# Kernel tuning notes

Measured on AMD Instinct MI355X. Metric: run time of the kernel, lower is better.

The kernel has to match this reference:

```python
import jax, jax.numpy as jnp
import numpy as np

H = 16      # q heads
G = 4       # groups (n_rep)
THETA = 10000.0


def _rope(x, cos, sin):
    # x pairs adjacent elements (torch complex view of reshape(..., -1, 2))
    x0 = x[..., ::2]
    x1 = x[..., 1::2]
    r0 = x0 * cos - x1 * sin
    r1 = x0 * sin + x1 * cos
    return jnp.stack([r0, r1], axis=-1).reshape(x.shape)


def setup_inputs() -> dict:
    key = jax.random.key(0)
    ks = jax.random.split(key, 5)
    B, S, D = 2, 2048, 1024
    return {
        "x": jax.random.normal(ks[0], (B, S, D), jnp.float32),
        "Wq": jax.random.normal(ks[1], (D, D), jnp.float32) * 0.02,
        "Wk": jax.random.normal(ks[2], (D, D // G), jnp.float32) * 0.02,
        "Wv": jax.random.normal(ks[3], (D, D // G), jnp.float32) * 0.02,
        "Wo": jax.random.normal(ks[4], (D, D), jnp.float32) * 0.02,
    }


def reference(x, Wq, Wk, Wv, Wo):
    B, S, D = x.shape
    hd = D // H                     # head dim = 64
    Hkv = H // G                    # kv heads = 4

    q = x @ Wq                      # (B,S,D)
    k = x @ Wk                      # (B,S,D/G)
    v = x @ Wv                      # (B,S,D/G)

    # repeat_kv: (B,S,Hkv,hd) -> (B,S,H,hd)
    k = jnp.repeat(k.reshape(B, S, Hkv, hd), G, axis=2)
    v = jnp.repeat(v.reshape(B, S, Hkv, hd), G, axis=2)

    # RoPE angles: freqs precomputed over hidden_dim (as in source)
    inv = 1.0 / (THETA ** (jnp.arange(0, D, 2, dtype=jnp.float32) / D))  # (D/2,)
    ang = jnp.arange(S, dtype=jnp.float32)[:, None] * inv[None, :]       # (S,D/2)
    q = _rope(q, jnp.cos(ang)[None], jnp.sin(ang)[None])                 # (B,S,D)
    angk = ang[:, : hd // 2]                                             # (S,hd/2)
    k = _rope(k, jnp.cos(angk)[None, :, None, :], jnp.sin(angk)[None, :, None, :])

    q = q.reshape(B, S, H, hd).transpose(0, 2, 1, 3)   # (B,H,S,hd)
    k = k.transpose(0, 2, 1, 3)
    v = v.transpose(0, 2, 1, 3)

    # NOTE: scale uses sqrt(hidden_dim), faithful to source
    scores = jnp.einsum('bhqd,bhkd->bhqk', q, k) / jnp.sqrt(jnp.float32(D))
    p = jax.nn.softmax(scores, axis=-1)
    o = jnp.einsum('bhqk,bhkd->bhqd', p, v)
    o = o.transpose(0, 2, 1, 3).reshape(B, S, D)
    return o @ Wo
```

## Files before the change

### kernel.cpp

```cpp
#include <hip/hip_runtime.h>
#include <math.h>

#define BATCH 2
#define SEQ   2048
#define DMODEL 1024
#define KDIM  1024
#define NH    16
#define HDIM  64
#define GRP   4
#define NKV   4
#define NSPLIT 2

enum { M_PLAIN = 0, M_QKV = 1 };

#define LN_THETA 9.210340371976184f
#define QSCALE 0.04508422002778f

typedef short bf8_t __attribute__((ext_vector_type(8)));
typedef float f4_t __attribute__((ext_vector_type(4)));
typedef unsigned short us4_t __attribute__((ext_vector_type(4)));
typedef unsigned short us8_t __attribute__((ext_vector_type(8)));
typedef _Float16 h_t;
typedef _Float16 h4_t __attribute__((ext_vector_type(4)));

#define QB_OFF 0
#define KB_OFF 4194304
#define VB_OFF (4194304 + 1048576)

__device__ __forceinline__ unsigned short f2bf(float f) {
  unsigned int u = __float_as_uint(f);
  u += 0x7fffu + ((u >> 16) & 1u);
  return (unsigned short)(u >> 16);
}

__device__ __forceinline__ float fexp2(float x) {
#if __has_builtin(__builtin_amdgcn_exp2f)
  return __builtin_amdgcn_exp2f(x);
#else
  return exp2f(x);
#endif
}

__device__ __forceinline__ void gload_lds16(const void* g, void* l) {
  typedef __attribute__((address_space(1))) unsigned int gu32;
  typedef __attribute__((address_space(3))) unsigned int lu32;
  __builtin_amdgcn_global_load_lds((const gu32*)g, (lu32*)l, 16, 0, 0);
}

__global__ __launch_bounds__(256) void conv_x(const float* __restrict__ in,
                                              unsigned short* __restrict__ out) {
  const int i = blockIdx.x * 256 + threadIdx.x;
  float4 v = ((const float4*)in)[i];
  us4_t o = {f2bf(v.x), f2bf(v.y), f2bf(v.z), f2bf(v.w)};
  ((us4_t*)out)[i] = o;
}

__global__ __launch_bounds__(256) void convT_all(const float* __restrict__ W0,
                                                 const float* __restrict__ W1,
                                                 const float* __restrict__ W2,
                                                 const float* __restrict__ W3,
                                                 unsigned short* __restrict__ Wqkvt,
                                                 unsigned short* __restrict__ Wot) {
  const float* W; unsigned short* out; int N, rowoff;
  switch (blockIdx.z) {
    case 0: W = W0; out = Wqkvt; N = 1024; rowoff = 0;    break;
    case 1: W = W1; out = Wqkvt; N = 256;  rowoff = 1024; break;
    case 2: W = W2; out = Wqkvt; N = 256;  rowoff = 1280; break;
    default: W = W3; out = Wot;  N = 1024; rowoff = 0;    break;
  }
  const int n0 = blockIdx.x * 64;
  if (n0 >= N) return;
  __shared__ unsigned short T[64][72];
  const int t = threadIdx.x;
  const int k0 = blockIdx.y * 64;
  const int kr = t >> 4, n4 = (t & 15) * 4;
#pragma unroll
  for (int i = 0; i < 4; ++i) {
    const int k = kr + i * 16;
    float4 v = *(const float4*)&W[(size_t)(k0 + k) * N + n0 + n4];
    T[n4 + 0][k] = f2bf(v.x);
    T[n4 + 1][k] = f2bf(v.y);
    T[n4 + 2][k] = f2bf(v.z);
    T[n4 + 3][k] = f2bf(v.w);
  }
  __syncthreads();
#pragma unroll
  for (int i = 0; i < 2; ++i) {
    const int c = t + i * 256;
    const int n = c >> 3, kc = (c & 7) * 8;
    us8_t v = *(const us8_t*)&T[n][kc];
    *(us8_t*)&out[(size_t)(rowoff + n0 + n) * KDIM + k0 + kc] = v;
  }
}

template <int MODE>
__global__ __launch_bounds__(512, 2) void gemm_bf16(const unsigned short* __restrict__ A,
                                                    const unsigned short* __restrict__ Bt,
                                                    void* __restrict__ Cdst_, int N) {
  __shared__ __align__(16) unsigned short As[4 * 4096];
  __shared__ __align__(16) unsigned short Bs[4 * 4096];

  const int tid = threadIdx.x;
  const int lane = tid & 63, quad = lane >> 4, l16 = lane & 15;
  const int w = tid >> 6, wm = w >> 1, wn = w & 1;
  const int row0 = blockIdx.x * 128, col0 = blockIdx.y * 128;

  const int m0 = tid >> 2;
  const int kc0 = (tid & 3) ^ ((m0 >> 1) & 3);
  const unsigned short* Ag0 = A + (size_t)(row0 + m0) * KDIM + kc0 * 8;
  const unsigned short* Bg0 = Bt + (size_t)(col0 + m0) * KDIM + kc0 * 8;
  unsigned short* Al0 = &As[tid * 8];
  unsigned short* Bl0 = &Bs[tid * 8];

#define STAGE_GEMM(kk)                                          \
  do {                                                          \
    _Pragma("unroll") for (int kh = 0; kh < 4; ++kh) {          \
      gload_lds16(Ag0 + (kk) + kh * 32, Al0 + kh * 4096);       \
      gload_lds16(Bg0 + (kk) + kh * 32, Bl0 + kh * 4096);       \
    }                                                           \
  } while (0)

  int aoff[2][4], boff[4][4];
#pragma unroll
  for (int mi = 0; mi < 2; ++mi) {
    const int am = wm * 32 + mi * 16 + l16;
    const int sw = quad ^ ((am >> 1) & 3);
#pragma unroll
    for (int kh = 0; kh < 4; ++kh)
      aoff[mi][kh] = kh * 4096 + (((am << 2) | sw) << 3);
  }
#pragma unroll
  for (int ni = 0; ni < 4; ++ni) {
    const int bn = wn * 64 + ni * 16 + l16;
    const int sw = quad ^ ((bn >> 1) & 3);
#pragma unroll
    for (int kh = 0; kh < 4; ++kh)
      boff[ni][kh] = kh * 4096 + (((bn << 2) | sw) << 3);
  }

  f4_t acc[2][4];
#pragma unroll
  for (int mi = 0; mi < 2; ++mi)
#pragma unroll
    for (int ni = 0; ni < 4; ++ni) acc[mi][ni] = (f4_t){0.f, 0.f, 0.f, 0.f};

  for (int kb = 0; kb < KDIM; kb += 128) {
    __syncthreads();
    STAGE_GEMM(kb);
    __syncthreads();

#pragma unroll
    for (int kh = 0; kh < 4; ++kh) {
      bf8_t af[2], bfr[4];
#pragma unroll
      for (int mi = 0; mi < 2; ++mi) af[mi] = *(const bf8_t*)&As[aoff[mi][kh]];
#pragma unroll
      for (int ni = 0; ni < 4; ++ni) bfr[ni] = *(const bf8_t*)&Bs[boff[ni][kh]];
#pragma unroll
      for (int mi = 0; mi < 2; ++mi)
#pragma unroll
        for (int ni = 0; ni < 4; ++ni)
          acc[mi][ni] = __builtin_amdgcn_mfma_f32_16x16x32_bf16(af[mi], bfr[ni], acc[mi][ni], 0, 0, 0);
    }
  }
#undef STAGE_GEMM

  if constexpr (MODE == M_PLAIN) {
    float* out = (float*)Cdst_;
#pragma unroll
    for (int mi = 0; mi < 2; ++mi) {
      const int rowb = row0 + wm * 32 + mi * 16 + quad * 4;
#pragma unroll
      for (int ni = 0; ni < 4; ++ni) {
        const int n = col0 + wn * 64 + ni * 16 + l16;
#pragma unroll
        for (int r = 0; r < 4; ++r)
          out[(size_t)(rowb + r) * N + n] = acc[mi][ni][r];
      }
    }
  } else {
    unsigned short* Qb = (unsigned short*)Cdst_;
    unsigned short* Kb = Qb + (KB_OFF - QB_OFF);
    unsigned short* Vb = Qb + (VB_OFF - QB_OFF);
#pragma unroll
    for (int ni = 0; ni < 4; ++ni) {
      const int nb = col0 + wn * 64 + ni * 16;
      const int n = nb + l16;
      if (nb < 1024) {
        const float inv = expf(-(float)(2 * (n >> 1)) * (LN_THETA / (float)DMODEL));
        const float sgn = (n & 1) ? 1.f : -1.f;
        const int h = n >> 6, d = n & 63;
#pragma unroll
        for (int mi = 0; mi < 2; ++mi) {
          const int rowb = row0 + wm * 32 + mi * 16 + quad * 4;
#pragma unroll
          for (int r = 0; r < 4; ++r) {
            const int row = rowb + r;
            const int bb = row >> 11, s = row & (SEQ - 1);
            const float v = acc[mi][ni][r];
            const float p = __shfl_xor(v, 1);
            float sn, cs;
            sincosf((float)s * inv, &sn, &cs);
            const float res = (v * cs + sgn * p * sn) * QSCALE;
            Qb[((size_t)(bb * NH + h) * SEQ + s) * HDIM + d] = f2bf(res);
          }
        }
      } else if (nb < 1280) {
        const int nk = n - 1024;
        const int hkv = nk >> 6, d = nk & 63;
        const float inv = expf(-(float)(2 * (d >> 1)) * (LN_THETA / (float)DMODEL));
        const float sgn = (nk & 1) ? 1.f : -1.f;
#pragma unroll
        for (int mi = 0; mi < 2; ++mi) {
          const int rowb = row0 + wm * 32 + mi * 16 + quad * 4;
#pragma unroll
          for (int r = 0; r < 4; ++r) {
            const int row = rowb + r;
            const int bb = row >> 11, s = row & (SEQ - 1);
            const float v = acc[mi][ni][r];
            const float p = __shfl_xor(v, 1);
            float sn, cs;
            sincosf((float)s * inv, &sn, &cs);
            const float res = v * cs + sgn * p * sn;
            Kb[((size_t)(bb * NKV + hkv) * SEQ + s) * HDIM + d] = f2bf(res);
          }
        }
      } else {
        const int nv = n - 1280;
        const int hkv = nv >> 6, d = nv & 63;
#pragma unroll
        for (int mi = 0; mi < 2; ++mi) {
          const int s0 = row0 + wm * 32 + mi * 16 + quad * 4;
          const int bb = s0 >> 11, sl = s0 & (SEQ - 1);
          const int st = sl & 63;
          const int ps = (sl & ~63) | (st & 0x20) | ((st & 0x0C) << 1) | ((st & 0x10) >> 2);
          us4_t stv = {f2bf(acc[mi][ni][0]), f2bf(acc[mi][ni][1]),
                       f2bf(acc[mi][ni][2]), f2bf(acc[mi][ni][3])};
          *(us4_t*)&Vb[((size_t)(bb * NKV + hkv) * HDIM + d) * SEQ + ps] = stv;
        }
      }
    }
  }
}

__global__ __launch_bounds__(256, 4) void attn_fwd(const unsigned short* __restrict__ Q,
                                                   const unsigned short* __restrict__ K,
                                                   const unsigned short* __restrict__ V,
                                                   h_t* __restrict__ Opart,
                                                   float* __restrict__ Lpart) {
  __shared__ __align__(16) unsigned short Kt[2 * 4096];
  __shared__ __align__(16) unsigned short Vt[2 * 4096];

  const int b = blockIdx.x >> 4;
  const int h = blockIdx.x & (NH - 1);
  const int hkv = h >> 2;
  const int q0 = blockIdx.y * 128;
  const int sp = blockIdx.z;
  const int tid = threadIdx.x;
  const int w = tid >> 6;
  const int lane = tid & 63;
  const int quad = lane >> 4;
  const int l16 = lane & 15;

  const unsigned short* Qg = Q + ((size_t)(b * NH + h) * SEQ + q0 + w * 32) * HDIM;
  const unsigned short* Kg = K + (size_t)(b * NKV + hkv) * SEQ * HDIM;
  const unsigned short* Vg = V + (size_t)(b * NKV + hkv) * HDIM * SEQ;

  bf8_t qb[2][2];
#pragma unroll
  for (int g = 0; g < 2; ++g)
#pragma unroll
    for (int half = 0; half < 2; ++half)
      qb[g][half] = *(const bf8_t*)(Qg + (size_t)(g * 16 + l16) * HDIM + half * 32 + quad * 8);

  f4_t accO[2][4];
#pragma unroll
  for (int g = 0; g < 2; ++g)
#pragma unroll
    for (int d = 0; d < 4; ++d) accO[g][d] = (f4_t){0.f, 0.f, 0.f, 0.f};
  float accLs[2] = {0.f, 0.f};

  const int sw8 = (quad ^ ((l16 >> 1) & 3)) << 3;

  const int skey = tid >> 2;
  const int gc = ((tid & 3) ^ ((tid >> 3) & 3)) << 3;
  const unsigned short* KgA = Kg + (size_t)skey * HDIM + gc;
  const unsigned short* VgA = Vg + (size_t)skey * SEQ + gc;

#define STAGE_ATTN(c, kk)                                                          \
  do {                                                                             \
    gload_lds16(KgA + (size_t)(kk) * HDIM,      &Kt[(c) * 4096 + tid * 8]);        \
    gload_lds16(KgA + (size_t)(kk) * HDIM + 32, &Kt[(c) * 4096 + tid * 8 + 2048]); \
    gload_lds16(VgA + (kk),      &Vt[(c) * 4096 + tid * 8]);                       \
    gload_lds16(VgA + (kk) + 32, &Vt[(c) * 4096 + tid * 8 + 2048]);                \
  } while (0)

  const int kbeg = sp * (SEQ / NSPLIT);
  const int kend = kbeg + SEQ / NSPLIT;

  STAGE_ATTN(0, kbeg);
  __syncthreads();
  int cur = 0;
  for (int k0 = kbeg; k0 < kend; k0 += 64) {
    if (k0 + 64 < kend) STAGE_ATTN(cur ^ 1, k0 + 64);

    const unsigned short* Ktc = Kt + cur * 4096;
    const unsigned short* Vtc = Vt + cur * 4096;

    union { bf8_t bf; unsigned int dw[4]; } pa[2][2];
#pragma unroll
    for (int cb = 0; cb < 4; ++cb) {
      const int koff = (cb * 16 + l16) * 32 + sw8;
      bf8_t kf0 = *(const bf8_t*)&Ktc[koff];
      bf8_t kf1 = *(const bf8_t*)&Ktc[koff + 2048];
#pragma unroll
      for (int g = 0; g < 2; ++g) {
        f4_t s = (f4_t){0.f, 0.f, 0.f, 0.f};
        s = __builtin_amdgcn_mfma_f32_16x16x32_bf16(kf0, qb[g][0], s, 0, 0, 0);
        s = __builtin_amdgcn_mfma_f32_16x16x32_bf16(kf1, qb[g][1], s, 0, 0, 0);
        const float p0 = fexp2(s[0]), p1 = fexp2(s[1]);
        const float p2 = fexp2(s[2]), p3 = fexp2(s[3]);
        accLs[g] += (p0 + p1) + (p2 + p3);
        unsigned int w0, w1;
        asm("v_cvt_pk_bf16_f32 %0, %1, %2" : "=v"(w0) : "v"(p0), "v"(p1));
        asm("v_cvt_pk_bf16_f32 %0, %1, %2" : "=v"(w1) : "v"(p2), "v"(p3));
        pa[g][cb >> 1].dw[(cb & 1) * 2 + 0] = w0;
        pa[g][cb >> 1].dw[(cb & 1) * 2 + 1] = w1;
      }
    }

#pragma unroll
    for (int db = 0; db < 4; ++db) {
      const int voff = (db * 16 + l16) * 32 + sw8;
      bf8_t vf0 = *(const bf8_t*)&Vtc[voff];
      bf8_t vf1 = *(const bf8_t*)&Vtc[voff + 2048];
#pragma unroll
      for (int g = 0; g < 2; ++g) {
        accO[g][db] = __builtin_amdgcn_mfma_f32_16x16x32_bf16(pa[g][0].bf, vf0, accO[g][db], 0, 0, 0);
        accO[g][db] = __builtin_amdgcn_mfma_f32_16x16x32_bf16(pa[g][1].bf, vf1, accO[g][db], 0, 0, 0);
      }
    }

    __syncthreads();
    cur ^= 1;
  }
#undef STAGE_ATTN

#pragma unroll
  for (int g = 0; g < 2; ++g) {
    accLs[g] += __shfl_xor(accLs[g], 16);
    accLs[g] += __shfl_xor(accLs[g], 32);
  }

  h_t* Osp = Opart + (size_t)sp * BATCH * SEQ * NH * HDIM;
  float* Lsp = Lpart + (size_t)sp * BATCH * SEQ * NH;
#pragma unroll
  for (int g = 0; g < 2; ++g)
#pragma unroll
    for (int r = 0; r < 4; ++r) {
      const int q = q0 + w * 32 + g * 16 + quad * 4 + r;
      const size_t rowi = ((size_t)b * SEQ + q) * NH + h;
      h_t* op = Osp + rowi * HDIM;
#pragma unroll
      for (int db = 0; db < 4; ++db)
        op[db * 16 + l16] = (h_t)accO[g][db][r];
    }
  if (quad == 0) {
#pragma unroll
    for (int g = 0; g < 2; ++g) {
      const int q = q0 + w * 32 + g * 16 + l16;
      Lsp[((size_t)b * SEQ + q) * NH + h] = accLs[g];
    }
  }
}

__global__ __launch_bounds__(256) void attn_merge(const h_t* __restrict__ Opart,
                                                  const float* __restrict__ Lpart,
                                                  unsigned short* __restrict__ Ow) {
  const int idx = blockIdx.x * 256 + threadIdx.x;
  const int g = idx >> 4, j = (idx & 15) * 4;
  const size_t nq = (size_t)BATCH * SEQ * NH;
  float L = 0.f;
  float4 acc = make_float4(0.f, 0.f, 0.f, 0.f);
#pragma unroll
  for (int u = 0; u < NSPLIT; ++u) {
    L += Lpart[u * nq + g];
    h4_t o = *(const h4_t*)&Opart[((size_t)u * nq + g) * HDIM + j];
    acc.x += (float)o[0]; acc.y += (float)o[1];
    acc.z += (float)o[2]; acc.w += (float)o[3];
  }
  const float il = 1.0f / L;
  us4_t o = {f2bf(acc.x * il), f2bf(acc.y * il), f2bf(acc.z * il), f2bf(acc.w * il)};
  *(us4_t*)&Ow[(size_t)g * HDIM + j] = o;
}

extern "C" void kernel_launch(void* const* d_in, const int* in_sizes, int n_in,
                              void* d_out, int out_size, void* d_ws, size_t ws_size,
                              hipStream_t stream) {
  (void)in_sizes; (void)n_in; (void)out_size; (void)ws_size;
  const float* x  = (const float*)d_in[0];
  const float* Wq = (const float*)d_in[1];
  const float* Wk = (const float*)d_in[2];
  const float* Wv = (const float*)d_in[3];
  const float* Wo = (const float*)d_in[4];
  float* out = (float*)d_out;

  unsigned short* Qb    = (unsigned short*)d_ws;
  unsigned short* Kb    = Qb + 4194304;
  unsigned short* Vb    = Kb + 1048576;
  unsigned short* xb    = Vb + 1048576;
  unsigned short* Owb   = xb + 4194304;
  unsigned short* Wqkvt = Owb + 4194304;
  unsigned short* Wot   = Wqkvt + 1572864;
  h_t* Opart = (h_t*)(Wot + 1048576);
  float* Lpart = (float*)(Opart + (size_t)NSPLIT * 4194304);

  dim3 blk(256);
  conv_x<<<dim3(4096), blk, 0, stream>>>(x, xb);
  convT_all<<<dim3(16, 16, 4), blk, 0, stream>>>(Wq, Wk, Wv, Wo, Wqkvt, Wot);

  gemm_bf16<M_QKV><<<dim3(32, 12), dim3(512), 0, stream>>>(xb, Wqkvt, Qb, 1536);
  attn_fwd<<<dim3(BATCH * NH, SEQ / 128, NSPLIT), blk, 0, stream>>>(Qb, Kb, Vb, Opart, Lpart);
  attn_merge<<<dim3(4096), blk, 0, stream>>>(Opart, Lpart, Owb);
  gemm_bf16<M_PLAIN><<<dim3(32, 8), dim3(512), 0, stream>>>(Owb, Wot, out, DMODEL);
}
```

Measured before the change: 166.2 us.

## Fuse x bf16 conversion into QKV GEMM and drop attention split-K merge

The QKV GEMM now reads fp32 x directly and converts it to bf16 while staging into LDS, which removes the separate conv_x kernel and its bf16 round trip through memory. The attention kernel no longer splits keys into two halves; each block walks all keys, normalizes by the row sum itself and writes bf16 output, which eliminates the attn_merge kernel and the fp16 partial buffers. In exchange the A-tile loads in the QKV GEMM become synchronous register loads plus LDS stores instead of direct global-to-LDS loads, and the attention grid shrinks to 512 blocks, which lowers parallelism.

```diff
diff --git a/kernel.cpp b/kernel.cpp
--- a/kernel.cpp
+++ b/kernel.cpp
@@ -9,7 +9,6 @@
 #define HDIM  64
 #define GRP   4
 #define NKV   4
-#define NSPLIT 2
 
 enum { M_PLAIN = 0, M_QKV = 1 };
 
@@ -20,8 +19,6 @@
 typedef float f4_t __attribute__((ext_vector_type(4)));
 typedef unsigned short us4_t __attribute__((ext_vector_type(4)));
 typedef unsigned short us8_t __attribute__((ext_vector_type(8)));
-typedef _Float16 h_t;
-typedef _Float16 h4_t __attribute__((ext_vector_type(4)));
 
 #define QB_OFF 0
 #define KB_OFF 4194304
@@ -45,14 +42,6 @@
   typedef __attribute__((address_space(1))) unsigned int gu32;
   typedef __attribute__((address_space(3))) unsigned int lu32;
   __builtin_amdgcn_global_load_lds((const gu32*)g, (lu32*)l, 16, 0, 0);
-}
-
-__global__ __launch_bounds__(256) void conv_x(const float* __restrict__ in,
-                                              unsigned short* __restrict__ out) {
-  const int i = blockIdx.x * 256 + threadIdx.x;
-  float4 v = ((const float4*)in)[i];
-  us4_t o = {f2bf(v.x), f2bf(v.y), f2bf(v.z), f2bf(v.w)};
-  ((us4_t*)out)[i] = o;
 }
 
 __global__ __launch_bounds__(256) void convT_all(const float* __restrict__ W0,
@@ -94,7 +83,7 @@
 }
 
 template <int MODE>
-__global__ __launch_bounds__(512, 2) void gemm_bf16(const unsigned short* __restrict__ A,
+__global__ __launch_bounds__(512, 2) void gemm_bf16(const void* __restrict__ A_,
                                                     const unsigned short* __restrict__ Bt,
                                                     void* __restrict__ Cdst_, int N) {
   __shared__ __align__(16) unsigned short As[4 * 4096];
@@ -107,17 +96,26 @@
 
   const int m0 = tid >> 2;
   const int kc0 = (tid & 3) ^ ((m0 >> 1) & 3);
-  const unsigned short* Ag0 = A + (size_t)(row0 + m0) * KDIM + kc0 * 8;
+  const unsigned short* Ag0 = (const unsigned short*)A_ + (size_t)(row0 + m0) * KDIM + kc0 * 8;
+  const float*          Xg0 = (const float*)A_ + (size_t)(row0 + m0) * KDIM + kc0 * 8;
   const unsigned short* Bg0 = Bt + (size_t)(col0 + m0) * KDIM + kc0 * 8;
   unsigned short* Al0 = &As[tid * 8];
   unsigned short* Bl0 = &Bs[tid * 8];
 
-#define STAGE_GEMM(kk)                                          \
-  do {                                                          \
-    _Pragma("unroll") for (int kh = 0; kh < 4; ++kh) {          \
-      gload_lds16(Ag0 + (kk) + kh * 32, Al0 + kh * 4096);       \
-      gload_lds16(Bg0 + (kk) + kh * 32, Bl0 + kh * 4096);       \
-    }                                                           \
+#define STAGE_GEMM(kk)                                                   \
+  do {                                                                   \
+    _Pragma("unroll") for (int kh = 0; kh < 4; ++kh) {                   \
+      if constexpr (MODE == M_QKV) {                                     \
+        float4 a0 = *(const float4*)(Xg0 + (kk) + kh * 32);              \
+        float4 a1 = *(const float4*)(Xg0 + (kk) + kh * 32 + 4);          \
+        us8_t o8 = {f2bf(a0.x), f2bf(a0.y), f2bf(a0.z), f2bf(a0.w),      \
+                    f2bf(a1.x), f2bf(a1.y), f2bf(a1.z), f2bf(a1.w)};     \
+        *(us8_t*)(Al0 + kh * 4096) = o8;                                 \
+      } else {                                                           \
+        gload_lds16(Ag0 + (kk) + kh * 32, Al0 + kh * 4096);              \
+      }                                                                  \
+      gload_lds16(Bg0 + (kk) + kh * 32, Bl0 + kh * 4096);                \
+    }                                                                    \
   } while (0)
 
   int aoff[2][4], boff[4][4];
@@ -246,8 +244,7 @@
 __global__ __launch_bounds__(256, 4) void attn_fwd(const unsigned short* __restrict__ Q,
                                                    const unsigned short* __restrict__ K,
                                                    const unsigned short* __restrict__ V,
-                                                   h_t* __restrict__ Opart,
-                                                   float* __restrict__ Lpart) {
+                                                   unsigned short* __restrict__ Ow) {
   __shared__ __align__(16) unsigned short Kt[2 * 4096];
   __shared__ __align__(16) unsigned short Vt[2 * 4096];
 
@@ -255,7 +252,6 @@
   const int h = blockIdx.x & (NH - 1);
   const int hkv = h >> 2;
   const int q0 = blockIdx.y * 128;
-  const int sp = blockIdx.z;
   const int tid = threadIdx.x;
   const int w = tid >> 6;
   const int lane = tid & 63;
@@ -295,14 +291,11 @@
     gload_lds16(VgA + (kk) + 32, &Vt[(c) * 4096 + tid * 8 + 2048]);                \
   } while (0)
 
-  const int kbeg = sp * (SEQ / NSPLIT);
-  const int kend = kbeg + SEQ / NSPLIT;
-
-  STAGE_ATTN(0, kbeg);
+  STAGE_ATTN(0, 0);
   __syncthreads();
   int cur = 0;
-  for (int k0 = kbeg; k0 < kend; k0 += 64) {
-    if (k0 + 64 < kend) STAGE_ATTN(cur ^ 1, k0 + 64);
+  for (int k0 = 0; k0 < SEQ; k0 += 64) {
+    if (k0 + 64 < SEQ) STAGE_ATTN(cur ^ 1, k0 + 64);
 
     const unsigned short* Ktc = Kt + cur * 4096;
     const unsigned short* Vtc = Vt + cur * 4096;
@@ -351,47 +344,20 @@
     accLs[g] += __shfl_xor(accLs[g], 16);
     accLs[g] += __shfl_xor(accLs[g], 32);
   }
-
-  h_t* Osp = Opart + (size_t)sp * BATCH * SEQ * NH * HDIM;
-  float* Lsp = Lpart + (size_t)sp * BATCH * SEQ * NH;
+  const float il0 = 1.0f / accLs[0];
+  const float il1 = 1.0f / accLs[1];
+
 #pragma unroll
   for (int g = 0; g < 2; ++g)
 #pragma unroll
     for (int r = 0; r < 4; ++r) {
+      const float ilr = __shfl(g ? il1 : il0, quad * 4 + r);
       const int q = q0 + w * 32 + g * 16 + quad * 4 + r;
-      const size_t rowi = ((size_t)b * SEQ + q) * NH + h;
-      h_t* op = Osp + rowi * HDIM;
+      unsigned short* op = Ow + (((size_t)b * SEQ + q) * NH + h) * HDIM;
 #pragma unroll
       for (int db = 0; db < 4; ++db)
-        op[db * 16 + l16] = (h_t)accO[g][db][r];
-    }
-  if (quad == 0) {
-#pragma unroll
-    for (int g = 0; g < 2; ++g) {
-      const int q = q0 + w * 32 + g * 16 + l16;
-      Lsp[((size_t)b * SEQ + q) * NH + h] = accLs[g];
-    }
-  }
-}
-
-__global__ __launch_bounds__(256) void attn_merge(const h_t* __restrict__ Opart,
-                                                  const float* __restrict__ Lpart,
-                                                  unsigned short* __restrict__ Ow) {
-  const int idx = blockIdx.x * 256 + threadIdx.x;
-  const int g = idx >> 4, j = (idx & 15) * 4;
-  const size_t nq = (size_t)BATCH * SEQ * NH;
-  float L = 0.f;
-  float4 acc = make_float4(0.f, 0.f, 0.f, 0.f);
-#pragma unroll
-  for (int u = 0; u < NSPLIT; ++u) {
-    L += Lpart[u * nq + g];
-    h4_t o = *(const h4_t*)&Opart[((size_t)u * nq + g) * HDIM + j];
-    acc.x += (float)o[0]; acc.y += (float)o[1];
-    acc.z += (float)o[2]; acc.w += (float)o[3];
-  }
-  const float il = 1.0f / L;
-  us4_t o = {f2bf(acc.x * il), f2bf(acc.y * il), f2bf(acc.z * il), f2bf(acc.w * il)};
-  *(us4_t*)&Ow[(size_t)g * HDIM + j] = o;
+        op[db * 16 + l16] = f2bf(accO[g][db][r] * ilr);
+    }
 }
 
 extern "C" void kernel_launch(void* const* d_in, const int* in_sizes, int n_in,
@@ -408,19 +374,14 @@
   unsigned short* Qb    = (unsigned short*)d_ws;
   unsigned short* Kb    = Qb + 4194304;
   unsigned short* Vb    = Kb + 1048576;
-  unsigned short* xb    = Vb + 1048576;
-  unsigned short* Owb   = xb + 4194304;
+  unsigned short* Owb   = Vb + 1048576;
   unsigned short* Wqkvt = Owb + 4194304;
   unsigned short* Wot   = Wqkvt + 1572864;
-  h_t* Opart = (h_t*)(Wot + 1048576);
-  float* Lpart = (float*)(Opart + (size_t)NSPLIT * 4194304);
 
   dim3 blk(256);
-  conv_x<<<dim3(4096), blk, 0, stream>>>(x, xb);
   convT_all<<<dim3(16, 16, 4), blk, 0, stream>>>(Wq, Wk, Wv, Wo, Wqkvt, Wot);
 
-  gemm_bf16<M_QKV><<<dim3(32, 12), dim3(512), 0, stream>>>(xb, Wqkvt, Qb, 1536);
-  attn_fwd<<<dim3(BATCH * NH, SEQ / 128, NSPLIT), blk, 0, stream>>>(Qb, Kb, Vb, Opart, Lpart);
-  attn_merge<<<dim3(4096), blk, 0, stream>>>(Opart, Lpart, Owb);
+  gemm_bf16<M_QKV><<<dim3(32, 12), dim3(512), 0, stream>>>(x, Wqkvt, Qb, 1536);
+  attn_fwd<<<dim3(BATCH * NH, SEQ / 128), blk, 0, stream>>>(Qb, Kb, Vb, Owb);
   gemm_bf16<M_PLAIN><<<dim3(32, 8), dim3(512), 0, stream>>>(Owb, Wot, out, DMODEL);
 }
```

New measurement: 163.8 us. About the same (-1.4%).
